# Optimization experiments

Hardware: AMD Instinct MI355X
Metric: run time of the kernel (lower is better)

The kernel has to match this reference:

```python
import jax, jax.numpy as jnp
import numpy as np

B, N, PREV, PRED, H = 16, 64, 6, 30, 256
E = N * (N - 1)
BN_EPS = 1e-5


def _mlp(x, W1, b1, W2, b2, gamma, beta):
    # Two-layer ELU MLP with batch norm over flattened (batch*rows) dim.
    h = jax.nn.elu(x @ W1 + b1)
    h = jax.nn.elu(h @ W2 + b2)
    b, n, d = h.shape
    f = h.reshape(b * n, d)
    mu = f.mean(axis=0)
    var = f.var(axis=0)
    f = (f - mu) * jax.lax.rsqrt(var + BN_EPS) * gamma + beta
    return f.reshape(b, n, d)


def setup_inputs() -> dict:
    key = jax.random.key(0)
    ks = jax.random.split(key, 8)
    # fully-connected directed graph without self loops
    recv, send = np.where(~np.eye(N, dtype=bool))  # each [E]
    rel_rec = jnp.broadcast_to(jax.nn.one_hot(jnp.asarray(recv), N)[None], (B, E, N)).astype(jnp.float32)
    rel_send = jnp.broadcast_to(jax.nn.one_hot(jnp.asarray(send), N)[None], (B, E, N)).astype(jnp.float32)

    def xavier(k, shape):
        fan_in, fan_out = shape
        std = np.sqrt(2.0 / (fan_in + fan_out))
        return jax.random.normal(k, shape, jnp.float32) * std

    return {
        "prev_actor_centers": jax.random.normal(ks[0], (B, N, PREV, 2), jnp.float32) * 10.0,
        "rel_rec": rel_rec,
        "rel_send": rel_send,
        "W_traj": xavier(ks[1], (PREV * 2, H)),
        "b_traj": jnp.full((H,), 0.1, jnp.float32),
        "n2e_W1": xavier(ks[2], (2 * H, H)),
        "n2e_b1": jnp.full((H,), 0.1, jnp.float32),
        "n2e_W2": xavier(ks[3], (H, H)),
        "n2e_b2": jnp.full((H,), 0.1, jnp.float32),
        "n2e_gamma": jnp.ones((H,), jnp.float32),
        "n2e_beta": jnp.zeros((H,), jnp.float32),
        "e2n_W1": xavier(ks[4], (2 * H, H)),
        "e2n_b1": jnp.full((H,), 0.1, jnp.float32),
        "e2n_W2": xavier(ks[5], (H, H)),
        "e2n_b2": jnp.full((H,), 0.1, jnp.float32),
        "e2n_gamma": jnp.ones((H,), jnp.float32),
        "e2n_beta": jnp.zeros((H,), jnp.float32),
        "W_fuse": xavier(ks[6], (2 * H, H)),
        "b_fuse": jnp.full((H,), 0.1, jnp.float32),
        "W_pred": xavier(ks[7], (H, PRED * 2)),
        "b_pred": jnp.full((PRED * 2,), 0.1, jnp.float32),
    }


def reference(prev_actor_centers, rel_rec, rel_send,
              W_traj, b_traj,
              n2e_W1, n2e_b1, n2e_W2, n2e_b2, n2e_gamma, n2e_beta,
              e2n_W1, e2n_b1, e2n_W2, e2n_b2, e2n_gamma, e2n_beta,
              W_fuse, b_fuse, W_pred, b_pred):
    b, n, prev, _ = prev_actor_centers.shape
    # relative displacements, first step zero
    diffs = prev_actor_centers[:, :, 1:, :] - prev_actor_centers[:, :, :-1, :]
    rel_pos = jnp.concatenate([jnp.zeros((b, n, 1, 2), prev_actor_centers.dtype), diffs], axis=2)
    rel_pos = rel_pos.reshape(b, n, prev * 2)
    x = rel_pos @ W_traj + b_traj  # [b, n, H] node features

    # node2edge: gather via one-hot relation matmuls
    receivers = jnp.einsum('ben,bnh->beh', rel_rec, x)
    senders = jnp.einsum('ben,bnh->beh', rel_send, x)
    edges = jnp.concatenate([receivers, senders], axis=-1)  # [b, E, 2H]
    e = _mlp(edges, n2e_W1, n2e_b1, n2e_W2, n2e_b2, n2e_gamma, n2e_beta)

    # edge2node: degree-normalized scatter via transposed relation matmuls
    deg_rec = rel_rec.sum(axis=1)  # [b, n]
    deg_rec = deg_rec + (deg_rec == 0).astype(deg_rec.dtype)
    incoming = jnp.einsum('ben,beh->bnh', rel_rec, e) / deg_rec[..., None]
    deg_send = rel_send.sum(axis=1)
    deg_send = deg_send + (deg_send == 0).astype(deg_send.dtype)
    outgoing = jnp.einsum('ben,beh->bnh', rel_send, e) / deg_send[..., None]
    nodes = jnp.concatenate([incoming, outgoing], axis=-1)  # [b, n, 2H]
    m = _mlp(nodes, e2n_W1, e2n_b1, e2n_W2, e2n_b2, e2n_gamma, e2n_beta)

    fused = jnp.concatenate([x, m], axis=-1) @ W_fuse + b_fuse  # [b, n, H]
    rel = fused @ W_pred + b_pred  # [b, n, PRED*2]

    current_loc = prev_actor_centers[:, :, -1, :]  # [b, n, 2]
    current_loc = jnp.broadcast_to(current_loc[:, :, None, :], (b, n, PRED, 2)).reshape(b, n, PRED * 2)
    pos = jnp.cumsum(rel.reshape(b, n, PRED, 2), axis=2).reshape(b, n, PRED * 2) + current_loc
    return (rel, pos)
```

## Files before the change

kernel.cpp:

```cpp
#include <hip/hip_runtime.h>
#include <hip/hip_bf16.h>

#define BB 16
#define NN 64
#define PREVN 6
#define PREDN 30
#define HH 256
#define EE 4032
#define EROWS (BB*EE)
#define NROWS (BB*NN)

typedef short short8 __attribute__((ext_vector_type(8)));
typedef float f32x4 __attribute__((ext_vector_type(4)));

enum : int {
  OFF_STATS_E = 0,
  OFF_STATS_M = 1024,
  OFF_XRS     = 2048,
  F32_END     = 264192
};
enum : size_t {
  BO_W1TE  = 262144,
  BO_W2TE  = 393216,
  BO_W1TN  = 458752,
  BO_W2TN  = 589824,
  BO_WFT   = 655360,
  BO_WPT   = 786432,
  BO_NODES = 802816,
  BO_M2    = 1327104,
  BO_E2    = 1589248
};

__device__ __forceinline__ float eluf(float v) { return v > 0.f ? v : __expf(v) - 1.f; }

__device__ __forceinline__ void gl2lds16(const void* g, void* l) {
  __builtin_amdgcn_global_load_lds(
      (const __attribute__((address_space(1))) void*)g,
      (__attribute__((address_space(3))) void*)l, 16, 0, 0);
}

__device__ __forceinline__ float xembed(const float* __restrict__ centers,
                                        const float* __restrict__ Wt,
                                        const float* __restrict__ bt,
                                        int rr, int col) {
  const float* c = centers + rr * 12;
  float acc = bt[col];
  #pragma unroll
  for (int t = 0; t < 5; ++t) {
    float dx = c[(t+1)*2 + 0] - c[t*2 + 0];
    float dy = c[(t+1)*2 + 1] - c[t*2 + 1];
    acc += dx * Wt[(2 + 2*t)*HH + col] + dy * Wt[(3 + 2*t)*HH + col];
  }
  return acc;
}

struct PrepArgs {
  const float *n2e_W1, *n2e_W2, *e2n_W1, *e2n_W2, *W_fuse, *W_pred;
  float* stats;
  __hip_bfloat16 *w1te, *w2te, *w1tn, *w2tn, *wft, *wpt;
};

__global__ __launch_bounds__(256) void k_prep(PrepArgs a) {
  __shared__ float t[64][65];
  const int bid = blockIdx.x, tid = threadIdx.x;
  if (bid < 128) {
    const float* W; __hip_bfloat16* WT; int K, lb;
    if (bid < 32)      { W = a.n2e_W1; WT = a.w1te; K = 512; lb = bid; }
    else if (bid < 48) { W = a.n2e_W2; WT = a.w2te; K = 256; lb = bid - 32; }
    else if (bid < 80) { W = a.e2n_W1; WT = a.w1tn; K = 512; lb = bid - 48; }
    else if (bid < 96) { W = a.e2n_W2; WT = a.w2tn; K = 256; lb = bid - 80; }
    else               { W = a.W_fuse; WT = a.wft;  K = 512; lb = bid - 96; }
    int KB = K / 64;
    int k0 = (lb % KB) * 64, n0 = (lb / KB) * 64;
    int tx = tid & 63, ty = tid >> 6;
    #pragma unroll
    for (int i = 0; i < 16; ++i)
      t[ty + i*4][tx] = W[(size_t)(k0 + ty + i*4) * 256 + n0 + tx];
    __syncthreads();
    #pragma unroll
    for (int i = 0; i < 16; ++i)
      WT[(size_t)(n0 + ty + i*4) * K + k0 + tx] = __float2bfloat16(t[tx][ty + i*4]);
  } else if (bid < 192) {
    int idx = (bid - 128) * 256 + tid;
    int c = idx >> 8, k = idx & 255;
    a.wpt[idx] = __float2bfloat16(c < 60 ? a.W_pred[k * 60 + c] : 0.f);
  } else {
    a.stats[(bid - 192) * 256 + tid] = 0.f;
  }
}

__global__ __launch_bounds__(256) void k_xrs(
    const float* __restrict__ centers,
    const float* __restrict__ W_traj,
    const float* __restrict__ b_traj,
    const __hip_bfloat16* __restrict__ W1T,
    const float* __restrict__ b1,
    __hip_bfloat16* __restrict__ xrs) {
  __shared__ alignas(16) __hip_bfloat16 xls[32][264];
  const int tid = threadIdx.x;
  const int w = tid >> 6, lane = tid & 63;
  const int m16 = lane & 15, quad = lane >> 4;
  const int ko = quad * 8;
  const int half = blockIdx.x >> 5;
  const int row0 = (blockIdx.x & 31) * 32;
  const int colw = w * 64;
  __hip_bfloat16* dst = xrs + (size_t)half * 262144;

  #pragma unroll 4
  for (int r = 0; r < 32; ++r)
    xls[r][tid] = __float2bfloat16(xembed(centers, W_traj, b_traj, row0 + r, tid));
  __syncthreads();

  f32x4 acc[2][4];
  #pragma unroll
  for (int jt = 0; jt < 4; ++jt) {
    float bv = half ? 0.f : b1[colw + jt*16 + m16];
    #pragma unroll
    for (int mt = 0; mt < 2; ++mt) acc[mt][jt] = (f32x4){bv, bv, bv, bv};
  }
  #pragma unroll
  for (int ks = 0; ks < 8; ++ks) {
    short8 af[2], bf[4];
    #pragma unroll
    for (int mt = 0; mt < 2; ++mt)
      af[mt] = *reinterpret_cast<const short8*>(&xls[mt*16 + m16][ks*32 + ko]);
    #pragma unroll
    for (int jt = 0; jt < 4; ++jt)
      bf[jt] = *reinterpret_cast<const short8*>(
          W1T + (size_t)(colw + jt*16 + m16)*512 + half*256 + ks*32 + ko);
    #pragma unroll
    for (int mt = 0; mt < 2; ++mt)
      #pragma unroll
      for (int jt = 0; jt < 4; ++jt)
        acc[mt][jt] = __builtin_amdgcn_mfma_f32_16x16x32_bf16(af[mt], bf[jt],
                                                              acc[mt][jt], 0, 0, 0);
  }
  #pragma unroll
  for (int mt = 0; mt < 2; ++mt)
    #pragma unroll
    for (int jt = 0; jt < 4; ++jt)
      #pragma unroll
      for (int r = 0; r < 4; ++r)
        dst[(size_t)(row0 + mt*16 + quad*4 + r)*256 + colw + jt*16 + m16] =
            __float2bfloat16(acc[mt][jt][r]);
}

__global__ __launch_bounds__(256, 2) void k_mlp6(
    const __hip_bfloat16* __restrict__ xrs,
    const __hip_bfloat16* __restrict__ W2T,
    const float* __restrict__ b2,
    __hip_bfloat16* __restrict__ outp,
    float* __restrict__ stats) {
  __shared__ alignas(16) char reg1[33792];
  __shared__ alignas(16) __hip_bfloat16 h1s[64][264];
  __shared__ float sst[2][256];
  const int tid = threadIdx.x;
  const int w = tid >> 6, lane = tid & 63;
  const int m16 = lane & 15, quad = lane >> 4;
  const int ko = quad * 8;
  const int blk = blockIdx.x;
  const int bb = blk / 63, lb = blk - bb*63;
  const int row0 = blk * 64;
  const int n0 = (lb * 64) / 63;
  const int colw = w * 64;

  const char* xsb = (const char*)(xrs + 262144 + (size_t)bb*64*256);
  #pragma unroll
  for (int i = 0; i < 8; ++i) {
    int seg = w*8 + i;
    gl2lds16(xsb + seg*1024 + lane*16, reg1 + seg*1024);
  }
  if (w == 0)
    gl2lds16((const char*)(xrs + (size_t)(bb*64 + n0)*256) + lane*16, reg1 + 32768);
  sst[0][tid] = 0.f;
  sst[1][tid] = 0.f;
  __syncthreads();

  {
    const int ty = tid >> 7;
    const int c2 = (tid & 127) * 2;
    #pragma unroll 4
    for (int r2 = 0; r2 < 32; ++r2) {
      int r = ty*32 + r2;
      int e = lb*64 + r;
      int rc = e / 63; int jj = e - rc*63;
      int sd = jj + (jj >= rc ? 1 : 0);
      __hip_bfloat162 xa = *reinterpret_cast<const __hip_bfloat162*>(
          reg1 + 32768 + (rc - n0)*512 + c2*2);
      __hip_bfloat162 xs2 = *reinterpret_cast<const __hip_bfloat162*>(
          reg1 + sd*512 + c2*2);
      __hip_bfloat162 o;
      o.x = __float2bfloat16(eluf(__bfloat162float(xa.x) + __bfloat162float(xs2.x)));
      o.y = __float2bfloat16(eluf(__bfloat162float(xa.y) + __bfloat162float(xs2.y)));
      *reinterpret_cast<__hip_bfloat162*>(&h1s[r][c2]) = o;
    }
  }
  __syncthreads();

  f32x4 acc2[4][4];
  #pragma unroll
  for (int jt = 0; jt < 4; ++jt) {
    float bv = b2[colw + jt*16 + m16];
    #pragma unroll
    for (int mt = 0; mt < 4; ++mt) acc2[mt][jt] = (f32x4){bv, bv, bv, bv};
  }
  #pragma unroll
  for (int kt = 0; kt < 4; ++kt) {
    #pragma unroll
    for (int ks = 0; ks < 2; ++ks) {
      const int k0 = kt*64 + ks*32 + ko;
      short8 af[4], bf[4];
      #pragma unroll
      for (int jt = 0; jt < 4; ++jt)
        bf[jt] = *reinterpret_cast<const short8*>(
            W2T + (size_t)(colw + jt*16 + m16)*256 + k0);
      #pragma unroll
      for (int mt = 0; mt < 4; ++mt)
        af[mt] = *(const short8*)((const char*)h1s +
                     (size_t)(mt*16 + m16)*528 + k0*2);
      #pragma unroll
      for (int mt = 0; mt < 4; ++mt)
        #pragma unroll
        for (int jt = 0; jt < 4; ++jt)
          acc2[mt][jt] = __builtin_amdgcn_mfma_f32_16x16x32_bf16(af[mt], bf[jt],
                                                                 acc2[mt][jt], 0, 0, 0);
    }
  }
  __syncthreads();

  #pragma unroll
  for (int jt = 0; jt < 4; ++jt) {
    float ps = 0.f, pq = 0.f;
    #pragma unroll
    for (int mt = 0; mt < 4; ++mt)
      #pragma unroll
      for (int r = 0; r < 4; ++r) {
        float hv = eluf(acc2[mt][jt][r]);
        h1s[mt*16 + quad*4 + r][colw + jt*16 + m16] = __float2bfloat16(hv);
        ps += hv; pq += hv * hv;
      }
    atomicAdd(&sst[0][colw + jt*16 + m16], ps);
    atomicAdd(&sst[1][colw + jt*16 + m16], pq);
  }
  __syncthreads();

  atomicAdd(&stats[tid], sst[0][tid]);
  atomicAdd(&stats[256 + tid], sst[1][tid]);
  #pragma unroll
  for (int i = 0; i < 8; ++i) {
    int u = i*256 + tid;
    int r = u >> 5, c = (u & 31) * 8;
    *reinterpret_cast<uint4*>(outp + (size_t)(row0 + r)*HH + c) =
        *reinterpret_cast<const uint4*>(&h1s[r][c]);
  }
}

__global__ __launch_bounds__(256, 2) void k_mlp3n(
    const __hip_bfloat16* __restrict__ A,
    const __hip_bfloat16* __restrict__ W1T,
    const float* __restrict__ b1,
    const __hip_bfloat16* __restrict__ W2T,
    const float* __restrict__ b2,
    __hip_bfloat16* __restrict__ outp,
    float* __restrict__ stats) {
  __shared__ alignas(16) __hip_bfloat16 Wt[256 * 64];
  __shared__ alignas(16) __hip_bfloat16 At[16 * 64];
  __shared__ alignas(16) __hip_bfloat16 h1s[16][264];
  const int tid = threadIdx.x;
  const int w = tid >> 6, lane = tid & 63;
  const int m16 = lane & 15, quad = lane >> 4;
  const int ko = quad * 8;
  const int row0 = blockIdx.x * 16;
  const int colw = w * 64;
  const int csub = lane >> 3, jl = lane & 7;
  const int jsrc = jl ^ csub;
  const int swz0 = ((quad)     ^ (m16 & 7)) * 16;
  const int swz1 = ((quad + 4) ^ (m16 & 7)) * 16;

  const __hip_bfloat16 *ar0 = nullptr, *ar1 = nullptr;
  if (w < 2) {
    int r = w * 8 + csub;
    ar0 = A + (size_t)(row0 + r) * 512;
    ar1 = ar0 + 256;
  }

  f32x4 acc[4];
  #pragma unroll
  for (int jt = 0; jt < 4; ++jt) {
    float bv = b1[colw + jt*16 + m16];
    acc[jt] = (f32x4){bv, bv, bv, bv};
  }
  for (int kt = 0; kt < 8; ++kt) {
    const int k0 = kt * 64;
    #pragma unroll
    for (int i = 0; i < 8; ++i) {
      const __hip_bfloat16* gp = W1T + (size_t)(colw + i*8 + csub) * 512 + k0 + jsrc*8;
      gl2lds16(gp, (char*)Wt + w*8192 + i*1024);
    }
    if (w < 2) {
      const __hip_bfloat16* gp = (k0 < 256 ? ar0 + k0 : ar1 + (k0 - 256)) + jsrc*8;
      gl2lds16(gp, (char*)At + w*1024);
    }
    __syncthreads();
    #pragma unroll
    for (int ks = 0; ks < 2; ++ks) {
      const int sw = ks ? swz1 : swz0;
      short8 af = *(const short8*)((const char*)At + m16*128 + sw);
      short8 bf[4];
      #pragma unroll
      for (int jt = 0; jt < 4; ++jt)
        bf[jt] = *(const short8*)((const char*)Wt + (colw + jt*16 + m16)*128 + sw);
      #pragma unroll
      for (int jt = 0; jt < 4; ++jt)
        acc[jt] = __builtin_amdgcn_mfma_f32_16x16x32_bf16(af, bf[jt], acc[jt], 0, 0, 0);
    }
    __syncthreads();
  }
  #pragma unroll
  for (int jt = 0; jt < 4; ++jt)
    #pragma unroll
    for (int r = 0; r < 4; ++r)
      h1s[quad*4 + r][colw + jt*16 + m16] = __float2bfloat16(eluf(acc[jt][r]));
  __syncthreads();

  f32x4 acc2[4];
  #pragma unroll
  for (int jt = 0; jt < 4; ++jt) {
    float bv = b2[colw + jt*16 + m16];
    acc2[jt] = (f32x4){bv, bv, bv, bv};
  }
  #pragma unroll
  for (int kt = 0; kt < 4; ++kt) {
    #pragma unroll
    for (int ks = 0; ks < 2; ++ks) {
      const int k0 = kt*64 + ks*32 + ko;
      short8 af = *(const short8*)((const char*)h1s + (size_t)m16*528 + k0*2);
      short8 bf[4];
      #pragma unroll
      for (int jt = 0; jt < 4; ++jt)
        bf[jt] = *reinterpret_cast<const short8*>(
            W2T + (size_t)(colw + jt*16 + m16)*256 + k0);
      #pragma unroll
      for (int jt = 0; jt < 4; ++jt)
        acc2[jt] = __builtin_amdgcn_mfma_f32_16x16x32_bf16(af, bf[jt], acc2[jt], 0, 0, 0);
    }
  }
  __syncthreads();
  #pragma unroll
  for (int jt = 0; jt < 4; ++jt)
    #pragma unroll
    for (int r = 0; r < 4; ++r)
      h1s[quad*4 + r][colw + jt*16 + m16] = __float2bfloat16(eluf(acc2[jt][r]));
  __syncthreads();

  {
    float s = 0.f, q = 0.f;
    #pragma unroll 8
    for (int r = 0; r < 16; ++r) {
      float v = __bfloat162float(h1s[r][tid]);
      s += v; q += v * v;
    }
    atomicAdd(&stats[tid], s);
    atomicAdd(&stats[256 + tid], q);
  }
  #pragma unroll
  for (int i = 0; i < 2; ++i) {
    int u = i*256 + tid;
    int r = u >> 5, c = (u & 31) * 8;
    *reinterpret_cast<uint4*>(outp + (size_t)(row0 + r)*HH + c) =
        *reinterpret_cast<const uint4*>(&h1s[r][c]);
  }
}

__global__ __launch_bounds__(1024) void k_agg2(const __hip_bfloat16* __restrict__ e2,
                                               const float* __restrict__ st,
                                               const float* __restrict__ gam,
                                               const float* __restrict__ bet,
                                               __hip_bfloat16* __restrict__ nodes) {
  __shared__ float red[32][256];
  const int blk = blockIdx.x;
  const int bn = blk >> 1, half = blk & 1;
  const int b = bn >> 6, n = bn & 63;
  const int tid = threadIdx.x;
  const int c8 = (tid & 31) * 8;
  const int rg = tid >> 5;
  const __hip_bfloat16* base = e2 + (size_t)b * EE * HH;
  float s[8] = {0.f,0.f,0.f,0.f,0.f,0.f,0.f,0.f};
  for (int j = rg; j < 63; j += 32) {
    const __hip_bfloat16* rp;
    if (half == 0) {
      rp = base + (size_t)(n*63 + j)*HH;
    } else {
      int i = j + (j >= n ? 1 : 0);
      int e = i*63 + n - (n > i ? 1 : 0);
      rp = base + (size_t)e*HH;
    }
    union { uint4 u; __hip_bfloat16 h[8]; } v;
    v.u = *reinterpret_cast<const uint4*>(rp + c8);
    #pragma unroll
    for (int jj = 0; jj < 8; ++jj) s[jj] += __bfloat162float(v.h[jj]);
  }
  #pragma unroll
  for (int jj = 0; jj < 8; jj += 4)
    *reinterpret_cast<float4*>(&red[rg][c8 + jj]) =
        (float4){s[jj], s[jj+1], s[jj+2], s[jj+3]};
  __syncthreads();
  if (tid < 256) {
    float S = 0.f;
    #pragma unroll
    for (int r = 0; r < 32; ++r) S += red[r][tid];
    const float inv = 1.f / (float)EROWS;
    float mean = st[tid] * inv;
    float var  = fmaxf(st[256 + tid] * inv - mean*mean, 0.f);
    float a = gam[tid] * rsqrtf(var + 1e-5f);
    float c0 = bet[tid] - mean * a;
    nodes[(size_t)bn*512 + half*256 + tid] = __float2bfloat16(a * S * (1.f/63.f) + c0);
  }
}

__global__ __launch_bounds__(256) void k_head2(
    const float* __restrict__ centers,
    const float* __restrict__ W_traj,
    const float* __restrict__ b_traj,
    const __hip_bfloat16* __restrict__ m2,
    const float* __restrict__ stM,
    const float* __restrict__ gam,
    const float* __restrict__ bet,
    const __hip_bfloat16* __restrict__ WfT,
    const float* __restrict__ bfv,
    const __hip_bfloat16* __restrict__ WpT,
    const float* __restrict__ bp,
    float* __restrict__ out) {
  __shared__ alignas(16) __hip_bfloat16 xs[16][264];
  __shared__ alignas(16) __hip_bfloat16 hs[16][264];
  __shared__ float rl[16][64];
  __shared__ float bnA[256], bnC[256];
  const int tid = threadIdx.x;
  const int w = tid >> 6, lane = tid & 63;
  const int m16 = lane & 15, quad = lane >> 4;
  const int ko = quad * 8;
  const int row0 = blockIdx.x * 16;
  const int colw = w * 64;

  {
    const float inv = 1.f / (float)NROWS;
    float mean = stM[tid] * inv;
    float var  = fmaxf(stM[256 + tid] * inv - mean*mean, 0.f);
    float am = gam[tid] * rsqrtf(var + 1e-5f);
    bnA[tid] = am;
    bnC[tid] = bet[tid] - mean * am;
  }
  #pragma unroll
  for (int r = 0; r < 16; ++r)
    xs[r][tid] = __float2bfloat16(xembed(centers, W_traj, b_traj, row0 + r, tid));
  __syncthreads();

  f32x4 acc[4];
  #pragma unroll
  for (int jt = 0; jt < 4; ++jt) {
    float bv = bfv[colw + jt*16 + m16];
    acc[jt] = (f32x4){bv, bv, bv, bv};
  }
  #pragma unroll
  for (int ks = 0; ks < 16; ++ks) {
    short8 af;
    if (ks < 8) {
      af = *reinterpret_cast<const short8*>(&xs[m16][ks*32 + ko]);
    } else {
      int k0 = (ks - 8)*32 + ko;
      union { uint4 u; __hip_bfloat16 h[8]; } v;
      v.u = *reinterpret_cast<const uint4*>(m2 + (size_t)(row0 + m16)*256 + k0);
      union { short8 s8; __hip_bfloat16 h[8]; } o;
      #pragma unroll
      for (int j = 0; j < 8; ++j)
        o.h[j] = __float2bfloat16(bnA[k0+j] * __bfloat162float(v.h[j]) + bnC[k0+j]);
      af = o.s8;
    }
    short8 bf[4];
    #pragma unroll
    for (int jt = 0; jt < 4; ++jt)
      bf[jt] = *reinterpret_cast<const short8*>(
          WfT + (size_t)(colw + jt*16 + m16)*512 + ks*32 + ko);
    #pragma unroll
    for (int jt = 0; jt < 4; ++jt)
      acc[jt] = __builtin_amdgcn_mfma_f32_16x16x32_bf16(af, bf[jt], acc[jt], 0, 0, 0);
  }
  #pragma unroll
  for (int jt = 0; jt < 4; ++jt)
    #pragma unroll
    for (int r = 0; r < 4; ++r)
      hs[quad*4 + r][colw + jt*16 + m16] = __float2bfloat16(acc[jt][r]);
  __syncthreads();

  if (w == 0) {
    f32x4 acc2[4];
    #pragma unroll
    for (int jt = 0; jt < 4; ++jt) {
      int c = jt*16 + m16;
      float bv = (c < 60) ? bp[c] : 0.f;
      acc2[jt] = (f32x4){bv, bv, bv, bv};
    }
    #pragma unroll
    for (int ks = 0; ks < 8; ++ks) {
      short8 af = *reinterpret_cast<const short8*>(&hs[m16][ks*32 + ko]);
      short8 bf[4];
      #pragma unroll
      for (int jt = 0; jt < 4; ++jt)
        bf[jt] = *reinterpret_cast<const short8*>(
            WpT + (size_t)(jt*16 + m16)*256 + ks*32 + ko);
      #pragma unroll
      for (int jt = 0; jt < 4; ++jt)
        acc2[jt] = __builtin_amdgcn_mfma_f32_16x16x32_bf16(af, bf[jt], acc2[jt], 0, 0, 0);
    }
    #pragma unroll
    for (int jt = 0; jt < 4; ++jt) {
      int c = jt*16 + m16;
      #pragma unroll
      for (int r = 0; r < 4; ++r) {
        int lr = quad*4 + r;
        rl[lr][c] = acc2[jt][r];
        if (c < 60) out[(size_t)(row0 + lr)*60 + c] = acc2[jt][r];
      }
    }
  }
  __syncthreads();

  if (tid < 32) {
    int lr = tid >> 1, xy = tid & 1;
    int grow = row0 + lr;
    float run = centers[(size_t)(grow*PREVN + 5)*2 + xy];
    #pragma unroll
    for (int p = 0; p < PREDN; ++p) {
      run += rl[lr][2*p + xy];
      out[61440 + (size_t)grow*60 + 2*p + xy] = run;
    }
  }
}

extern "C" void kernel_launch(void* const* d_in, const int* in_sizes, int n_in,
                              void* d_out, int out_size, void* d_ws, size_t ws_size,
                              hipStream_t stream) {
  const float* centers = (const float*)d_in[0];
  float* ws = (float*)d_ws;
  __hip_bfloat16* wb = (__hip_bfloat16*)(ws + F32_END);
  __hip_bfloat16* xrs = (__hip_bfloat16*)(ws + OFF_XRS);

  const float* W_traj = (const float*)d_in[3];
  const float* b_traj = (const float*)d_in[4];
  const float* n2e_b1 = (const float*)d_in[6];
  const float* n2e_b2 = (const float*)d_in[8];
  const float* n2e_g  = (const float*)d_in[9];
  const float* n2e_be = (const float*)d_in[10];
  const float* e2n_b1 = (const float*)d_in[12];
  const float* e2n_b2 = (const float*)d_in[14];
  const float* e2n_g  = (const float*)d_in[15];
  const float* e2n_be = (const float*)d_in[16];
  const float* b_fuse = (const float*)d_in[18];
  const float* b_pred = (const float*)d_in[20];

  PrepArgs pa;
  pa.n2e_W1 = (const float*)d_in[5];  pa.n2e_W2 = (const float*)d_in[7];
  pa.e2n_W1 = (const float*)d_in[11]; pa.e2n_W2 = (const float*)d_in[13];
  pa.W_fuse = (const float*)d_in[17]; pa.W_pred = (const float*)d_in[19];
  pa.stats = ws;
  pa.w1te = wb + BO_W1TE; pa.w2te = wb + BO_W2TE;
  pa.w1tn = wb + BO_W1TN; pa.w2tn = wb + BO_W2TN;
  pa.wft = wb + BO_WFT;   pa.wpt = wb + BO_WPT;

  k_prep<<<200, 256, 0, stream>>>(pa);
  k_xrs<<<64, 256, 0, stream>>>(centers, W_traj, b_traj, wb + BO_W1TE, n2e_b1, xrs);
  k_mlp6<<<EROWS/64, 256, 0, stream>>>(xrs, wb + BO_W2TE, n2e_b2,
                                       wb + BO_E2, ws + OFF_STATS_E);
  k_agg2<<<2*NROWS, 1024, 0, stream>>>(wb + BO_E2, ws + OFF_STATS_E, n2e_g, n2e_be,
                                       wb + BO_NODES);
  k_mlp3n<<<NROWS/16, 256, 0, stream>>>(wb + BO_NODES, wb + BO_W1TN, e2n_b1,
                                        wb + BO_W2TN, e2n_b2,
                                        wb + BO_M2, ws + OFF_STATS_M);
  k_head2<<<NROWS/16, 256, 0, stream>>>(centers, W_traj, b_traj, wb + BO_M2,
                                        ws + OFF_STATS_M, e2n_g, e2n_be,
                                        wb + BO_WFT, b_fuse, wb + BO_WPT, b_pred,
                                        (float*)d_out);
}
```

Baseline: 206.3 us.

## Split node MLP and head into fine-grained single-wave kernels across more blocks

Replaces the fused node-MLP kernel and the fused fuse/pred head kernel with four separate kernels (first layer, second layer with BN stats, fuse layer, pred plus cumsum). Each runs as many single-wave 64-thread blocks that each own a 16-row by 64-column tile, so the small node stage is spread over more compute units. The x embedding is now written to global once in k_xrs and reused by the fuse kernel instead of being recomputed. In exchange it adds launches and global round-trips for the intermediate activations, and the workspace layout is reshuffled.

```diff
diff --git a/kernel.cpp b/kernel.cpp
--- a/kernel.cpp
+++ b/kernel.cpp
@@ -20,15 +20,18 @@
   F32_END     = 264192
 };
 enum : size_t {
-  BO_W1TE  = 262144,
-  BO_W2TE  = 393216,
-  BO_W1TN  = 458752,
-  BO_W2TN  = 589824,
-  BO_WFT   = 655360,
-  BO_WPT   = 786432,
+  BO_W1TE  = 0,
+  BO_W2TE  = 131072,
+  BO_W1TN  = 196608,
+  BO_W2TN  = 327680,
+  BO_WFT   = 393216,
+  BO_WPT   = 524288,
+  BO_XG    = 540672,
   BO_NODES = 802816,
-  BO_M2    = 1327104,
-  BO_E2    = 1589248
+  BO_H1G   = 1327104,
+  BO_M2    = 1589248,
+  BO_FG    = 1851392,
+  BO_E2    = 2113536
 };
 
 __device__ __forceinline__ float eluf(float v) { return v > 0.f ? v : __expf(v) - 1.f; }
@@ -56,7 +59,7 @@
 
 struct PrepArgs {
   const float *n2e_W1, *n2e_W2, *e2n_W1, *e2n_W2, *W_fuse, *W_pred;
-  float* stats;
+  float* ws;
   __hip_bfloat16 *w1te, *w2te, *w1tn, *w2tn, *wft, *wpt;
 };
 
@@ -85,7 +88,7 @@
     int c = idx >> 8, k = idx & 255;
     a.wpt[idx] = __float2bfloat16(c < 60 ? a.W_pred[k * 60 + c] : 0.f);
   } else {
-    a.stats[(bid - 192) * 256 + tid] = 0.f;
+    a.ws[(bid - 192) * 256 + tid] = 0.f;
   }
 }
 
@@ -95,7 +98,8 @@
     const float* __restrict__ b_traj,
     const __hip_bfloat16* __restrict__ W1T,
     const float* __restrict__ b1,
-    __hip_bfloat16* __restrict__ xrs) {
+    __hip_bfloat16* __restrict__ xrs,
+    __hip_bfloat16* __restrict__ xg) {
   __shared__ alignas(16) __hip_bfloat16 xls[32][264];
   const int tid = threadIdx.x;
   const int w = tid >> 6, lane = tid & 63;
@@ -110,6 +114,16 @@
   for (int r = 0; r < 32; ++r)
     xls[r][tid] = __float2bfloat16(xembed(centers, W_traj, b_traj, row0 + r, tid));
   __syncthreads();
+
+  if (half == 0) {
+    #pragma unroll
+    for (int i = 0; i < 4; ++i) {
+      int u = i*256 + tid;
+      int r = u >> 5, c = (u & 31) * 8;
+      *reinterpret_cast<uint4*>(xg + (size_t)(row0 + r)*256 + c) =
+          *reinterpret_cast<const uint4*>(&xls[r][c]);
+    }
+  }
 
   f32x4 acc[2][4];
   #pragma unroll
@@ -248,123 +262,6 @@
   atomicAdd(&stats[256 + tid], sst[1][tid]);
   #pragma unroll
   for (int i = 0; i < 8; ++i) {
-    int u = i*256 + tid;
-    int r = u >> 5, c = (u & 31) * 8;
-    *reinterpret_cast<uint4*>(outp + (size_t)(row0 + r)*HH + c) =
-        *reinterpret_cast<const uint4*>(&h1s[r][c]);
-  }
-}
-
-__global__ __launch_bounds__(256, 2) void k_mlp3n(
-    const __hip_bfloat16* __restrict__ A,
-    const __hip_bfloat16* __restrict__ W1T,
-    const float* __restrict__ b1,
-    const __hip_bfloat16* __restrict__ W2T,
-    const float* __restrict__ b2,
-    __hip_bfloat16* __restrict__ outp,
-    float* __restrict__ stats) {
-  __shared__ alignas(16) __hip_bfloat16 Wt[256 * 64];
-  __shared__ alignas(16) __hip_bfloat16 At[16 * 64];
-  __shared__ alignas(16) __hip_bfloat16 h1s[16][264];
-  const int tid = threadIdx.x;
-  const int w = tid >> 6, lane = tid & 63;
-  const int m16 = lane & 15, quad = lane >> 4;
-  const int ko = quad * 8;
-  const int row0 = blockIdx.x * 16;
-  const int colw = w * 64;
-  const int csub = lane >> 3, jl = lane & 7;
-  const int jsrc = jl ^ csub;
-  const int swz0 = ((quad)     ^ (m16 & 7)) * 16;
-  const int swz1 = ((quad + 4) ^ (m16 & 7)) * 16;
-
-  const __hip_bfloat16 *ar0 = nullptr, *ar1 = nullptr;
-  if (w < 2) {
-    int r = w * 8 + csub;
-    ar0 = A + (size_t)(row0 + r) * 512;
-    ar1 = ar0 + 256;
-  }
-
-  f32x4 acc[4];
-  #pragma unroll
-  for (int jt = 0; jt < 4; ++jt) {
-    float bv = b1[colw + jt*16 + m16];
-    acc[jt] = (f32x4){bv, bv, bv, bv};
-  }
-  for (int kt = 0; kt < 8; ++kt) {
-    const int k0 = kt * 64;
-    #pragma unroll
-    for (int i = 0; i < 8; ++i) {
-      const __hip_bfloat16* gp = W1T + (size_t)(colw + i*8 + csub) * 512 + k0 + jsrc*8;
-      gl2lds16(gp, (char*)Wt + w*8192 + i*1024);
-    }
-    if (w < 2) {
-      const __hip_bfloat16* gp = (k0 < 256 ? ar0 + k0 : ar1 + (k0 - 256)) + jsrc*8;
-      gl2lds16(gp, (char*)At + w*1024);
-    }
-    __syncthreads();
-    #pragma unroll
-    for (int ks = 0; ks < 2; ++ks) {
-      const int sw = ks ? swz1 : swz0;
-      short8 af = *(const short8*)((const char*)At + m16*128 + sw);
-      short8 bf[4];
-      #pragma unroll
-      for (int jt = 0; jt < 4; ++jt)
-        bf[jt] = *(const short8*)((const char*)Wt + (colw + jt*16 + m16)*128 + sw);
-      #pragma unroll
-      for (int jt = 0; jt < 4; ++jt)
-        acc[jt] = __builtin_amdgcn_mfma_f32_16x16x32_bf16(af, bf[jt], acc[jt], 0, 0, 0);
-    }
-    __syncthreads();
-  }
-  #pragma unroll
-  for (int jt = 0; jt < 4; ++jt)
-    #pragma unroll
-    for (int r = 0; r < 4; ++r)
-      h1s[quad*4 + r][colw + jt*16 + m16] = __float2bfloat16(eluf(acc[jt][r]));
-  __syncthreads();
-
-  f32x4 acc2[4];
-  #pragma unroll
-  for (int jt = 0; jt < 4; ++jt) {
-    float bv = b2[colw + jt*16 + m16];
-    acc2[jt] = (f32x4){bv, bv, bv, bv};
-  }
-  #pragma unroll
-  for (int kt = 0; kt < 4; ++kt) {
-    #pragma unroll
-    for (int ks = 0; ks < 2; ++ks) {
-      const int k0 = kt*64 + ks*32 + ko;
-      short8 af = *(const short8*)((const char*)h1s + (size_t)m16*528 + k0*2);
-      short8 bf[4];
-      #pragma unroll
-      for (int jt = 0; jt < 4; ++jt)
-        bf[jt] = *reinterpret_cast<const short8*>(
-            W2T + (size_t)(colw + jt*16 + m16)*256 + k0);
-      #pragma unroll
-      for (int jt = 0; jt < 4; ++jt)
-        acc2[jt] = __builtin_amdgcn_mfma_f32_16x16x32_bf16(af, bf[jt], acc2[jt], 0, 0, 0);
-    }
-  }
-  __syncthreads();
-  #pragma unroll
-  for (int jt = 0; jt < 4; ++jt)
-    #pragma unroll
-    for (int r = 0; r < 4; ++r)
-      h1s[quad*4 + r][colw + jt*16 + m16] = __float2bfloat16(eluf(acc2[jt][r]));
-  __syncthreads();
-
-  {
-    float s = 0.f, q = 0.f;
-    #pragma unroll 8
-    for (int r = 0; r < 16; ++r) {
-      float v = __bfloat162float(h1s[r][tid]);
-      s += v; q += v * v;
-    }
-    atomicAdd(&stats[tid], s);
-    atomicAdd(&stats[256 + tid], q);
-  }
-  #pragma unroll
-  for (int i = 0; i < 2; ++i) {
     int u = i*256 + tid;
     int r = u >> 5, c = (u & 31) * 8;
     *reinterpret_cast<uint4*>(outp + (size_t)(row0 + r)*HH + c) =
@@ -418,54 +315,152 @@
   }
 }
 
-__global__ __launch_bounds__(256) void k_head2(
-    const float* __restrict__ centers,
-    const float* __restrict__ W_traj,
-    const float* __restrict__ b_traj,
+__global__ __launch_bounds__(64) void k_n1(
+    const __hip_bfloat16* __restrict__ nodes,
+    const __hip_bfloat16* __restrict__ W1T,
+    const float* __restrict__ b1,
+    __hip_bfloat16* __restrict__ h1g) {
+  __shared__ alignas(16) __hip_bfloat16 hls[16][72];
+  const int lane = threadIdx.x;
+  const int m16 = lane & 15, quad = lane >> 4;
+  const int ko = quad * 8;
+  const int row0 = (blockIdx.x >> 2) * 16;
+  const int j0 = (blockIdx.x & 3) * 64;
+
+  f32x4 acc[4];
+  #pragma unroll
+  for (int jt = 0; jt < 4; ++jt) {
+    float bv = b1[j0 + jt*16 + m16];
+    acc[jt] = (f32x4){bv, bv, bv, bv};
+  }
+  #pragma unroll
+  for (int ks = 0; ks < 16; ++ks) {
+    short8 af = *reinterpret_cast<const short8*>(
+        nodes + (size_t)(row0 + m16)*512 + ks*32 + ko);
+    short8 bf[4];
+    #pragma unroll
+    for (int jt = 0; jt < 4; ++jt)
+      bf[jt] = *reinterpret_cast<const short8*>(
+          W1T + (size_t)(j0 + jt*16 + m16)*512 + ks*32 + ko);
+    #pragma unroll
+    for (int jt = 0; jt < 4; ++jt)
+      acc[jt] = __builtin_amdgcn_mfma_f32_16x16x32_bf16(af, bf[jt], acc[jt], 0, 0, 0);
+  }
+  #pragma unroll
+  for (int jt = 0; jt < 4; ++jt)
+    #pragma unroll
+    for (int r = 0; r < 4; ++r)
+      hls[quad*4 + r][jt*16 + m16] = __float2bfloat16(eluf(acc[jt][r]));
+  #pragma unroll
+  for (int i = 0; i < 2; ++i) {
+    int u = i*64 + lane;
+    int r = u >> 3, c = (u & 7) * 8;
+    *reinterpret_cast<uint4*>(h1g + (size_t)(row0 + r)*256 + j0 + c) =
+        *reinterpret_cast<const uint4*>(&hls[r][c]);
+  }
+}
+
+__global__ __launch_bounds__(64) void k_n2(
+    const __hip_bfloat16* __restrict__ h1g,
+    const __hip_bfloat16* __restrict__ W2T,
+    const float* __restrict__ b2,
+    __hip_bfloat16* __restrict__ m2,
+    float* __restrict__ stats) {
+  __shared__ alignas(16) __hip_bfloat16 hls[16][72];
+  __shared__ float sst[2][64];
+  const int lane = threadIdx.x;
+  const int m16 = lane & 15, quad = lane >> 4;
+  const int ko = quad * 8;
+  const int row0 = (blockIdx.x >> 2) * 16;
+  const int j0 = (blockIdx.x & 3) * 64;
+
+  sst[0][lane] = 0.f;
+  sst[1][lane] = 0.f;
+
+  f32x4 acc[4];
+  #pragma unroll
+  for (int jt = 0; jt < 4; ++jt) {
+    float bv = b2[j0 + jt*16 + m16];
+    acc[jt] = (f32x4){bv, bv, bv, bv};
+  }
+  #pragma unroll
+  for (int ks = 0; ks < 8; ++ks) {
+    short8 af = *reinterpret_cast<const short8*>(
+        h1g + (size_t)(row0 + m16)*256 + ks*32 + ko);
+    short8 bf[4];
+    #pragma unroll
+    for (int jt = 0; jt < 4; ++jt)
+      bf[jt] = *reinterpret_cast<const short8*>(
+          W2T + (size_t)(j0 + jt*16 + m16)*256 + ks*32 + ko);
+    #pragma unroll
+    for (int jt = 0; jt < 4; ++jt)
+      acc[jt] = __builtin_amdgcn_mfma_f32_16x16x32_bf16(af, bf[jt], acc[jt], 0, 0, 0);
+  }
+  #pragma unroll
+  for (int jt = 0; jt < 4; ++jt) {
+    float ps = 0.f, pq = 0.f;
+    #pragma unroll
+    for (int r = 0; r < 4; ++r) {
+      float hv = eluf(acc[jt][r]);
+      hls[quad*4 + r][jt*16 + m16] = __float2bfloat16(hv);
+      ps += hv; pq += hv * hv;
+    }
+    atomicAdd(&sst[0][jt*16 + m16], ps);
+    atomicAdd(&sst[1][jt*16 + m16], pq);
+  }
+  atomicAdd(&stats[j0 + lane], sst[0][lane]);
+  atomicAdd(&stats[256 + j0 + lane], sst[1][lane]);
+  #pragma unroll
+  for (int i = 0; i < 2; ++i) {
+    int u = i*64 + lane;
+    int r = u >> 3, c = (u & 7) * 8;
+    *reinterpret_cast<uint4*>(m2 + (size_t)(row0 + r)*256 + j0 + c) =
+        *reinterpret_cast<const uint4*>(&hls[r][c]);
+  }
+}
+
+__global__ __launch_bounds__(64) void k_hf(
+    const __hip_bfloat16* __restrict__ xg,
     const __hip_bfloat16* __restrict__ m2,
     const float* __restrict__ stM,
     const float* __restrict__ gam,
     const float* __restrict__ bet,
     const __hip_bfloat16* __restrict__ WfT,
     const float* __restrict__ bfv,
-    const __hip_bfloat16* __restrict__ WpT,
-    const float* __restrict__ bp,
-    float* __restrict__ out) {
-  __shared__ alignas(16) __hip_bfloat16 xs[16][264];
-  __shared__ alignas(16) __hip_bfloat16 hs[16][264];
-  __shared__ float rl[16][64];
+    __hip_bfloat16* __restrict__ fg) {
+  __shared__ alignas(16) __hip_bfloat16 hls[16][72];
   __shared__ float bnA[256], bnC[256];
-  const int tid = threadIdx.x;
-  const int w = tid >> 6, lane = tid & 63;
+  const int lane = threadIdx.x;
   const int m16 = lane & 15, quad = lane >> 4;
   const int ko = quad * 8;
-  const int row0 = blockIdx.x * 16;
-  const int colw = w * 64;
+  const int row0 = (blockIdx.x >> 2) * 16;
+  const int j0 = (blockIdx.x & 3) * 64;
 
   {
     const float inv = 1.f / (float)NROWS;
-    float mean = stM[tid] * inv;
-    float var  = fmaxf(stM[256 + tid] * inv - mean*mean, 0.f);
-    float am = gam[tid] * rsqrtf(var + 1e-5f);
-    bnA[tid] = am;
-    bnC[tid] = bet[tid] - mean * am;
-  }
-  #pragma unroll
-  for (int r = 0; r < 16; ++r)
-    xs[r][tid] = __float2bfloat16(xembed(centers, W_traj, b_traj, row0 + r, tid));
-  __syncthreads();
+    #pragma unroll
+    for (int j = 0; j < 4; ++j) {
+      int k = lane*4 + j;
+      float mean = stM[k] * inv;
+      float var  = fmaxf(stM[256 + k] * inv - mean*mean, 0.f);
+      float am = gam[k] * rsqrtf(var + 1e-5f);
+      bnA[k] = am;
+      bnC[k] = bet[k] - mean * am;
+    }
+  }
 
   f32x4 acc[4];
   #pragma unroll
   for (int jt = 0; jt < 4; ++jt) {
-    float bv = bfv[colw + jt*16 + m16];
+    float bv = bfv[j0 + jt*16 + m16];
     acc[jt] = (f32x4){bv, bv, bv, bv};
   }
   #pragma unroll
   for (int ks = 0; ks < 16; ++ks) {
     short8 af;
     if (ks < 8) {
-      af = *reinterpret_cast<const short8*>(&xs[m16][ks*32 + ko]);
+      af = *reinterpret_cast<const short8*>(
+          xg + (size_t)(row0 + m16)*256 + ks*32 + ko);
     } else {
       int k0 = (ks - 8)*32 + ko;
       union { uint4 u; __hip_bfloat16 h[8]; } v;
@@ -480,7 +475,7 @@
     #pragma unroll
     for (int jt = 0; jt < 4; ++jt)
       bf[jt] = *reinterpret_cast<const short8*>(
-          WfT + (size_t)(colw + jt*16 + m16)*512 + ks*32 + ko);
+          WfT + (size_t)(j0 + jt*16 + m16)*512 + ks*32 + ko);
     #pragma unroll
     for (int jt = 0; jt < 4; ++jt)
       acc[jt] = __builtin_amdgcn_mfma_f32_16x16x32_bf16(af, bf[jt], acc[jt], 0, 0, 0);
@@ -489,44 +484,60 @@
   for (int jt = 0; jt < 4; ++jt)
     #pragma unroll
     for (int r = 0; r < 4; ++r)
-      hs[quad*4 + r][colw + jt*16 + m16] = __float2bfloat16(acc[jt][r]);
-  __syncthreads();
-
-  if (w == 0) {
-    f32x4 acc2[4];
-    #pragma unroll
-    for (int jt = 0; jt < 4; ++jt) {
-      int c = jt*16 + m16;
-      float bv = (c < 60) ? bp[c] : 0.f;
-      acc2[jt] = (f32x4){bv, bv, bv, bv};
-    }
-    #pragma unroll
-    for (int ks = 0; ks < 8; ++ks) {
-      short8 af = *reinterpret_cast<const short8*>(&hs[m16][ks*32 + ko]);
-      short8 bf[4];
-      #pragma unroll
-      for (int jt = 0; jt < 4; ++jt)
-        bf[jt] = *reinterpret_cast<const short8*>(
-            WpT + (size_t)(jt*16 + m16)*256 + ks*32 + ko);
-      #pragma unroll
-      for (int jt = 0; jt < 4; ++jt)
-        acc2[jt] = __builtin_amdgcn_mfma_f32_16x16x32_bf16(af, bf[jt], acc2[jt], 0, 0, 0);
-    }
-    #pragma unroll
-    for (int jt = 0; jt < 4; ++jt) {
-      int c = jt*16 + m16;
-      #pragma unroll
-      for (int r = 0; r < 4; ++r) {
-        int lr = quad*4 + r;
-        rl[lr][c] = acc2[jt][r];
-        if (c < 60) out[(size_t)(row0 + lr)*60 + c] = acc2[jt][r];
-      }
-    }
-  }
-  __syncthreads();
-
-  if (tid < 32) {
-    int lr = tid >> 1, xy = tid & 1;
+      hls[quad*4 + r][jt*16 + m16] = __float2bfloat16(acc[jt][r]);
+  #pragma unroll
+  for (int i = 0; i < 2; ++i) {
+    int u = i*64 + lane;
+    int r = u >> 3, c = (u & 7) * 8;
+    *reinterpret_cast<uint4*>(fg + (size_t)(row0 + r)*256 + j0 + c) =
+        *reinterpret_cast<const uint4*>(&hls[r][c]);
+  }
+}
+
+__global__ __launch_bounds__(64) void k_pred(
+    const __hip_bfloat16* __restrict__ fg,
+    const __hip_bfloat16* __restrict__ WpT,
+    const float* __restrict__ bp,
+    const float* __restrict__ centers,
+    float* __restrict__ out) {
+  __shared__ float rl[16][68];
+  const int lane = threadIdx.x;
+  const int m16 = lane & 15, quad = lane >> 4;
+  const int ko = quad * 8;
+  const int row0 = blockIdx.x * 16;
+
+  f32x4 acc[4];
+  #pragma unroll
+  for (int jt = 0; jt < 4; ++jt) {
+    int c = jt*16 + m16;
+    float bv = (c < 60) ? bp[c] : 0.f;
+    acc[jt] = (f32x4){bv, bv, bv, bv};
+  }
+  #pragma unroll
+  for (int ks = 0; ks < 8; ++ks) {
+    short8 af = *reinterpret_cast<const short8*>(
+        fg + (size_t)(row0 + m16)*256 + ks*32 + ko);
+    short8 bf[4];
+    #pragma unroll
+    for (int jt = 0; jt < 4; ++jt)
+      bf[jt] = *reinterpret_cast<const short8*>(
+          WpT + (size_t)(jt*16 + m16)*256 + ks*32 + ko);
+    #pragma unroll
+    for (int jt = 0; jt < 4; ++jt)
+      acc[jt] = __builtin_amdgcn_mfma_f32_16x16x32_bf16(af, bf[jt], acc[jt], 0, 0, 0);
+  }
+  #pragma unroll
+  for (int jt = 0; jt < 4; ++jt) {
+    int c = jt*16 + m16;
+    #pragma unroll
+    for (int r = 0; r < 4; ++r) {
+      int lr = quad*4 + r;
+      rl[lr][c] = acc[jt][r];
+      if (c < 60) out[(size_t)(row0 + lr)*60 + c] = acc[jt][r];
+    }
+  }
+  if (lane < 32) {
+    int lr = lane >> 1, xy = lane & 1;
     int grow = row0 + lr;
     float run = centers[(size_t)(grow*PREVN + 5)*2 + xy];
     #pragma unroll
@@ -562,22 +573,23 @@
   pa.n2e_W1 = (const float*)d_in[5];  pa.n2e_W2 = (const float*)d_in[7];
   pa.e2n_W1 = (const float*)d_in[11]; pa.e2n_W2 = (const float*)d_in[13];
   pa.W_fuse = (const float*)d_in[17]; pa.W_pred = (const float*)d_in[19];
-  pa.stats = ws;
+  pa.ws = ws;
   pa.w1te = wb + BO_W1TE; pa.w2te = wb + BO_W2TE;
   pa.w1tn = wb + BO_W1TN; pa.w2tn = wb + BO_W2TN;
   pa.wft = wb + BO_WFT;   pa.wpt = wb + BO_WPT;
 
   k_prep<<<200, 256, 0, stream>>>(pa);
-  k_xrs<<<64, 256, 0, stream>>>(centers, W_traj, b_traj, wb + BO_W1TE, n2e_b1, xrs);
-  k_mlp6<<<EROWS/64, 256, 0, stream>>>(xrs, wb + BO_W2TE, n2e_b2,
-                                       wb + BO_E2, ws + OFF_STATS_E);
+  k_xrs<<<64, 256, 0, stream>>>(centers, W_traj, b_traj, wb + BO_W1TE, n2e_b1,
+                                xrs, wb + BO_XG);
+  k_mlp6<<<EROWS/64, 256, 0, stream>>>(xrs, wb + BO_W2TE, n2e_b2, wb + BO_E2,
+                                       ws + OFF_STATS_E);
   k_agg2<<<2*NROWS, 1024, 0, stream>>>(wb + BO_E2, ws + OFF_STATS_E, n2e_g, n2e_be,
                                        wb + BO_NODES);
-  k_mlp3n<<<NROWS/16, 256, 0, stream>>>(wb + BO_NODES, wb + BO_W1TN, e2n_b1,
-                                        wb + BO_W2TN, e2n_b2,
-                                        wb + BO_M2, ws + OFF_STATS_M);
-  k_head2<<<NROWS/16, 256, 0, stream>>>(centers, W_traj, b_traj, wb + BO_M2,
-                                        ws + OFF_STATS_M, e2n_g, e2n_be,
-                                        wb + BO_WFT, b_fuse, wb + BO_WPT, b_pred,
-                                        (float*)d_out);
-}
+  k_n1<<<256, 64, 0, stream>>>(wb + BO_NODES, wb + BO_W1TN, e2n_b1, wb + BO_H1G);
+  k_n2<<<256, 64, 0, stream>>>(wb + BO_H1G, wb + BO_W2TN, e2n_b2, wb + BO_M2,
+                               ws + OFF_STATS_M);
+  k_hf<<<256, 64, 0, stream>>>(wb + BO_XG, wb + BO_M2, ws + OFF_STATS_M,
+                               e2n_g, e2n_be, wb + BO_WFT, b_fuse, wb + BO_FG);
+  k_pred<<<64, 64, 0, stream>>>(wb + BO_FG, wb + BO_WPT, b_pred, centers,
+                                (float*)d_out);
+}
```

Result: faster. 201.7 us (-2.2%).
